# Kernel tuning notes

Hardware: AMD Instinct MI355X
Metric: run time of the kernel (lower is better)

Reference implementation:

```python
import jax, jax.numpy as jnp
import numpy as np

B, IN_DIM, EXP_DIM, E = 16384, 256, 128, 8  # batch, input_dim, expert_dim, expert_num


def setup_inputs() -> dict:
    key = jax.random.key(0)
    ks = jax.random.split(key, 12)
    s_in = 1.0 / np.sqrt(IN_DIM)
    return {
        "x_a": jax.random.normal(ks[0], (B, IN_DIM), jnp.float32),
        "x_b": jax.random.normal(ks[1], (B, IN_DIM), jnp.float32),
        "x_share": jax.random.normal(ks[2], (B, IN_DIM), jnp.float32),
        # expert banks: [E, IN_DIM, EXP_DIM] weights, [E, EXP_DIM] bias
        "Wa": jax.random.uniform(ks[3], (E, IN_DIM, EXP_DIM), jnp.float32, -s_in, s_in),
        "ba": jax.random.uniform(ks[4], (E, EXP_DIM), jnp.float32, -s_in, s_in),
        "Wb": jax.random.uniform(ks[5], (E, IN_DIM, EXP_DIM), jnp.float32, -s_in, s_in),
        "bb": jax.random.uniform(ks[6], (E, EXP_DIM), jnp.float32, -s_in, s_in),
        "Ws": jax.random.uniform(ks[7], (E, IN_DIM, EXP_DIM), jnp.float32, -s_in, s_in),
        "bs": jax.random.uniform(ks[8], (E, EXP_DIM), jnp.float32, -s_in, s_in),
        # gate projections (bias=False): num single-output linears == one [num, IN_DIM] matrix
        "Ga": jax.random.uniform(ks[9], (2 * E, IN_DIM), jnp.float32, -s_in, s_in),
        "Gb": jax.random.uniform(ks[10], (2 * E, IN_DIM), jnp.float32, -s_in, s_in),
        "Gs": jax.random.uniform(ks[11], (3 * E, IN_DIM), jnp.float32, -s_in, s_in),
    }


def _experts(x, W, b):
    # batched dense stack: [B,IN] x [E,IN,D] -> [B,E,D]
    return jnp.einsum("bi,eid->bed", x, W) + b[None, :, :]


def _gate(x, G, experts):
    # logits [B, num]; softmax over experts; weighted sum over expert axis
    w = jax.nn.softmax(x @ G.T, axis=1)
    return jnp.einsum("be,bed->bd", w, experts)


def reference(x_a, x_b, x_share, Wa, ba, Wb, bb, Ws, bs, Ga, Gb, Gs):
    ea = _experts(x_a, Wa, ba)          # [B,E,D]
    eb = _experts(x_b, Wb, bb)          # [B,E,D]
    es = _experts(x_share, Ws, bs)      # [B,E,D]
    out_a = _gate(x_a, Ga, jnp.concatenate([ea, es], axis=1))
    out_b = _gate(x_b, Gb, jnp.concatenate([eb, es], axis=1))
    out_s = _gate(x_share, Gs, jnp.concatenate([ea, eb, es], axis=1))
    return (out_a, out_b, out_s)
```

## Files before the change

kernel.cpp:

```cpp
#include <hip/hip_runtime.h>
#include <stdint.h>

#define BATCH 16384
#define INDIM 256
#define DDIM  128
#define NEXP  8
#define ROWS  64
#define THREADS 512
#define NH    48
#define SLABE 16384

typedef __bf16 bfv8  __attribute__((ext_vector_type(8)));
typedef float  f32x4 __attribute__((ext_vector_type(4)));

typedef __attribute__((address_space(1))) const void gas_void;
typedef __attribute__((address_space(3))) void las_void;

__global__ void prep_kernel(const float* __restrict__ Wa, const float* __restrict__ Wb,
                            const float* __restrict__ Ws, const float* __restrict__ Ga,
                            const float* __restrict__ Gb, const float* __restrict__ Gs,
                            __bf16* __restrict__ wp, __bf16* __restrict__ gp) {
    int t = blockIdx.x * 256 + threadIdx.x;
    const int NW = 3 * 8 * 8 * 8 * 64;
    if (t < NW) {
        int lane = t & 63, nt = (t >> 6) & 7, kt = (t >> 9) & 7, e = (t >> 12) & 7, st = t >> 15;
        const float* W = (st == 0) ? Wa : (st == 1) ? Wb : Ws;
        int d  = nt * 16 + (lane & 15);
        int i0 = kt * 32 + (lane >> 4) * 8;
        __bf16* o = wp + (size_t)t * 8;
#pragma unroll
        for (int j = 0; j < 8; j++)
            o[j] = (__bf16)W[(size_t)(e * 256 + i0 + j) * 128 + d];
    } else if (t < NW + 2048) {
        int t2 = t - NW;
        int lane = t2 & 63, nt = (t2 >> 6) & 3, kt = t2 >> 8;
        int g  = nt * 16 + (lane & 15);
        int k0 = kt * 32 + (lane >> 4) * 8;
        __bf16* o = gp + (size_t)t2 * 8;
#pragma unroll
        for (int j = 0; j < 8; j++) {
            int k = k0 + j;
            float v = 0.f;
            if (g < 16)      v = Ga[g * 256 + k];
            else if (g < 32) v = Gb[(g - 16) * 256 + k];
            else if (g < 56) v = Gs[(g - 32) * 256 + k];
            o[j] = (__bf16)v;
        }
    }
}

__device__ __forceinline__ void load_afr(const float* __restrict__ x, int rb,
                                         int l16, int quad, bfv8 afr[2][8]) {
#pragma unroll
    for (int mt = 0; mt < 2; mt++) {
        const float* xr = x + (size_t)(rb + mt * 16 + l16) * INDIM;
#pragma unroll
        for (int kt = 0; kt < 8; kt++) {
            const f32x4* p = (const f32x4*)(xr + kt * 32 + quad * 8);
            f32x4 lo = __builtin_nontemporal_load(p);
            f32x4 hi = __builtin_nontemporal_load(p + 1);
            bfv8 a;
            a[0] = (__bf16)lo[0]; a[1] = (__bf16)lo[1]; a[2] = (__bf16)lo[2]; a[3] = (__bf16)lo[3];
            a[4] = (__bf16)hi[0]; a[5] = (__bf16)hi[1]; a[6] = (__bf16)hi[2]; a[7] = (__bf16)hi[3];
            afr[mt][kt] = a;
        }
    }
}

__device__ __forceinline__ void stage_half(const __bf16* __restrict__ wp,
                                           __bf16* ring, int h, int wv, int lane) {
    const __bf16* src = wp + ((size_t)h << 14) + (wv << 11) + (lane << 3);
    __bf16* dst = ring + ((h & 1) << 14) + (wv << 11);
#pragma unroll
    for (int i = 0; i < 4; i++)
        __builtin_amdgcn_global_load_lds((gas_void*)(src + (i << 9)),
                                         (las_void*)(dst + (i << 9)), 16, 0, 0);
}

__launch_bounds__(THREADS, 2)
__global__ void ple_kernel(const float* __restrict__ xa, const float* __restrict__ xb,
                           const float* __restrict__ xs,
                           const float* __restrict__ ba, const float* __restrict__ bb,
                           const float* __restrict__ bs,
                           const __bf16* __restrict__ wp, const __bf16* __restrict__ gp,
                           float* __restrict__ out) {
    __shared__ __bf16 ring[2 * SLABE];
    __shared__ float lgt[ROWS * 64];
    __shared__ float wT[64 * ROWS];

    const int tid  = threadIdx.x;
    const int wv   = tid >> 6;
    const int lane = tid & 63;
    const int rg   = wv >> 2;
    const int cg   = wv & 3;
    const int quad = lane >> 4;
    const int l16  = lane & 15;
    const int r0   = blockIdx.x * ROWS;
    const int rb   = r0 + rg * 32;

    stage_half(wp, ring, 0, wv, lane);

    bfv8 afr[2][8];

    {
        const float* x = (cg == 0) ? xa : (cg == 1) ? xb : xs;
        load_afr(x, rb, l16, quad, afr);
        f32x4 acc1[2];
#pragma unroll
        for (int mt = 0; mt < 2; mt++) { f32x4 z = {0.f, 0.f, 0.f, 0.f}; acc1[mt] = z; }
#pragma unroll
        for (int kt = 0; kt < 8; kt++) {
            bfv8 gfr = *(const bfv8*)(gp + ((size_t)(kt * 4 + cg) * 64 + lane) * 8);
#pragma unroll
            for (int mt = 0; mt < 2; mt++)
                acc1[mt] = __builtin_amdgcn_mfma_f32_16x16x32_bf16(afr[mt][kt], gfr, acc1[mt], 0, 0, 0);
        }
#pragma unroll
        for (int mt = 0; mt < 2; mt++)
#pragma unroll
            for (int r = 0; r < 4; r++)
                lgt[(rg * 32 + mt * 16 + quad * 4 + r) * 64 + cg * 16 + l16] = acc1[mt][r];
    }
    __syncthreads();

    if (tid < ROWS) {
        const float* L = lgt + tid * 64;
#pragma unroll
        for (int gi = 0; gi < 3; gi++) {
            const int base = (gi == 0) ? 0 : (gi == 1 ? 16 : 32);
            const int cnt  = (gi == 2) ? 24 : 16;
            float m = -1e30f;
            for (int k = 0; k < cnt; k++) m = fmaxf(m, L[base + k]);
            float s = 0.f;
            for (int k = 0; k < cnt; k++) s += __expf(L[base + k] - m);
            float inv = 1.f / s;
            for (int k = 0; k < cnt; k++) wT[(base + k) * ROWS + tid] = __expf(L[base + k] - m) * inv;
        }
    }
    __syncthreads();

    float o[3][2][2][4];
#pragma unroll
    for (int oi = 0; oi < 3; oi++)
#pragma unroll
        for (int mt = 0; mt < 2; mt++)
#pragma unroll
            for (int ntl = 0; ntl < 2; ntl++)
#pragma unroll
                for (int r = 0; r < 4; r++) o[oi][mt][ntl][r] = 0.f;

#define FOLD(oi, gbase)                                                                 \
    {                                                                                   \
        _Pragma("unroll")                                                               \
        for (int mt = 0; mt < 2; mt++) {                                                \
            f32x4 gw4 = *(const f32x4*)(wT + (gbase + eb) * ROWS + rg * 32 + mt * 16 + quad * 4); \
            _Pragma("unroll")                                                           \
            for (int ntl = 0; ntl < 2; ntl++)                                           \
                _Pragma("unroll")                                                       \
                for (int r = 0; r < 4; r++)                                             \
                    o[oi][mt][ntl][r] += gw4[r] * acc[mt][ntl][r];                      \
        }                                                                               \
    }

#pragma unroll
    for (int st = 0; st < 3; st++) {
        const float* x    = (st == 0) ? xa : (st == 1) ? xb : xs;
        const float* bias = (st == 0) ? ba : (st == 1) ? bb : bs;
        load_afr(x, rb, l16, quad, afr);

#pragma unroll 1
        for (int eb = 0; eb < NEXP; eb++) {
            float b0 = bias[eb * 128 + cg * 32 + l16];
            float b1 = bias[eb * 128 + cg * 32 + 16 + l16];

            f32x4 acc[2][2];
#pragma unroll
            for (int mt = 0; mt < 2; mt++)
#pragma unroll
                for (int ntl = 0; ntl < 2; ntl++) { f32x4 z = {0.f, 0.f, 0.f, 0.f}; acc[mt][ntl] = z; }

#pragma unroll
            for (int half = 0; half < 2; half++) {
                const int h = st * 16 + eb * 2 + half;
                __syncthreads();
                if (h + 1 < NH)
                    stage_half(wp, ring, h + 1, wv, lane);

                const __bf16* buf = ring + (half << 14);
#pragma unroll
                for (int kt4 = 0; kt4 < 4; kt4++) {
                    const int kt = half * 4 + kt4;
                    const __bf16* slab = buf + (kt4 << 12) + (cg << 10);
                    bfv8 bv0 = *(const bfv8*)(slab + ((size_t)lane << 3));
                    bfv8 bv1 = *(const bfv8*)(slab + 512 + ((size_t)lane << 3));
                    acc[0][0] = __builtin_amdgcn_mfma_f32_16x16x32_bf16(afr[0][kt], bv0, acc[0][0], 0, 0, 0);
                    acc[1][0] = __builtin_amdgcn_mfma_f32_16x16x32_bf16(afr[1][kt], bv0, acc[1][0], 0, 0, 0);
                    acc[0][1] = __builtin_amdgcn_mfma_f32_16x16x32_bf16(afr[0][kt], bv1, acc[0][1], 0, 0, 0);
                    acc[1][1] = __builtin_amdgcn_mfma_f32_16x16x32_bf16(afr[1][kt], bv1, acc[1][1], 0, 0, 0);
                }
            }

#pragma unroll
            for (int mt = 0; mt < 2; mt++)
#pragma unroll
                for (int r = 0; r < 4; r++) { acc[mt][0][r] += b0; acc[mt][1][r] += b1; }

            if (st == 0)      { FOLD(0, 0);  FOLD(2, 32); }
            else if (st == 1) { FOLD(1, 16); FOLD(2, 40); }
            else              { FOLD(0, 8);  FOLD(1, 24); FOLD(2, 48); }
        }
    }
#undef FOLD

#pragma unroll
    for (int oi = 0; oi < 3; oi++) {
        float* ob = out + (size_t)oi * BATCH * DDIM;
#pragma unroll
        for (int mt = 0; mt < 2; mt++)
#pragma unroll
            for (int r = 0; r < 4; r++) {
                int row = rb + mt * 16 + quad * 4 + r;
#pragma unroll
                for (int ntl = 0; ntl < 2; ntl++)
                    __builtin_nontemporal_store(o[oi][mt][ntl][r],
                        &ob[(size_t)row * DDIM + cg * 32 + ntl * 16 + l16]);
            }
    }
}

extern "C" void kernel_launch(void* const* d_in, const int* in_sizes, int n_in,
                              void* d_out, int out_size, void* d_ws, size_t ws_size,
                              hipStream_t stream) {
    const float* xa = (const float*)d_in[0];
    const float* xb = (const float*)d_in[1];
    const float* xs = (const float*)d_in[2];
    const float* Wa = (const float*)d_in[3];
    const float* ba = (const float*)d_in[4];
    const float* Wb = (const float*)d_in[5];
    const float* bb = (const float*)d_in[6];
    const float* Ws = (const float*)d_in[7];
    const float* bs = (const float*)d_in[8];
    const float* Ga = (const float*)d_in[9];
    const float* Gb = (const float*)d_in[10];
    const float* Gs = (const float*)d_in[11];

    __bf16* wp = (__bf16*)d_ws;
    __bf16* gp = wp + 3 * 8 * 8 * 8 * 64 * 8;

    prep_kernel<<<392, 256, 0, stream>>>(Wa, Wb, Ws, Ga, Gb, Gs, wp, gp);
    ple_kernel<<<BATCH / ROWS, THREADS, 0, stream>>>(xa, xb, xs, ba, bb, bs, wp, gp, (float*)d_out);
}
```

Before: 186.6 us.

## Coalesce weight repack via LDS transpose and rotate expert order per block

Result: faster. 180.7 us (-3.2%).

```diff
diff --git a/kernel.cpp b/kernel.cpp
--- a/kernel.cpp
+++ b/kernel.cpp
@@ -7,7 +7,7 @@
 #define NEXP  8
 #define ROWS  64
 #define THREADS 512
-#define NH    48
+#define NSEQ  48
 #define SLABE 16384
 
 typedef __bf16 bfv8  __attribute__((ext_vector_type(8)));
@@ -20,19 +20,38 @@
                             const float* __restrict__ Ws, const float* __restrict__ Ga,
                             const float* __restrict__ Gb, const float* __restrict__ Gs,
                             __bf16* __restrict__ wp, __bf16* __restrict__ gp) {
-    int t = blockIdx.x * 256 + threadIdx.x;
-    const int NW = 3 * 8 * 8 * 8 * 64;
-    if (t < NW) {
-        int lane = t & 63, nt = (t >> 6) & 7, kt = (t >> 9) & 7, e = (t >> 12) & 7, st = t >> 15;
+    __shared__ float ws[32 * 132];
+    const int b = blockIdx.x, tid = threadIdx.x;
+    if (b < 192) {
+        const int st = b >> 6, e = (b >> 3) & 7, kt = b & 7;
         const float* W = (st == 0) ? Wa : (st == 1) ? Wb : Ws;
-        int d  = nt * 16 + (lane & 15);
-        int i0 = kt * 32 + (lane >> 4) * 8;
-        __bf16* o = wp + (size_t)t * 8;
-#pragma unroll
-        for (int j = 0; j < 8; j++)
-            o[j] = (__bf16)W[(size_t)(e * 256 + i0 + j) * 128 + d];
-    } else if (t < NW + 2048) {
-        int t2 = t - NW;
+        const float* src = W + (size_t)(e * 256 + kt * 32) * 128;
+#pragma unroll
+        for (int k = 0; k < 4; k++) {
+            int idx4 = tid + k * 256;
+            f32x4 v = *(const f32x4*)(src + (size_t)idx4 * 4);
+            int row = idx4 >> 5;
+            int col = (idx4 & 31) << 2;
+            ws[row * 132 + col + 0] = v[0];
+            ws[row * 132 + col + 1] = v[1];
+            ws[row * 132 + col + 2] = v[2];
+            ws[row * 132 + col + 3] = v[3];
+        }
+        __syncthreads();
+        __bf16* o = wp + ((size_t)b << 12);
+#pragma unroll
+        for (int h2 = 0; h2 < 2; h2++) {
+            int base = tid * 2 + h2;
+            int nt = base >> 6, lane = base & 63;
+            int d  = nt * 16 + (lane & 15);
+            int i0 = (lane >> 4) * 8;
+            bfv8 ov;
+#pragma unroll
+            for (int j = 0; j < 8; j++) ov[j] = (__bf16)ws[(i0 + j) * 132 + d];
+            *(bfv8*)(o + (size_t)base * 8) = ov;
+        }
+    } else {
+        int t2 = (b - 192) * 256 + tid;
         int lane = t2 & 63, nt = (t2 >> 6) & 3, kt = t2 >> 8;
         int g  = nt * 16 + (lane & 15);
         int k0 = kt * 32 + (lane >> 4) * 8;
@@ -67,14 +86,21 @@
     }
 }
 
-__device__ __forceinline__ void stage_half(const __bf16* __restrict__ wp,
-                                           __bf16* ring, int h, int wv, int lane) {
-    const __bf16* src = wp + ((size_t)h << 14) + (wv << 11) + (lane << 3);
-    __bf16* dst = ring + ((h & 1) << 14) + (wv << 11);
+__device__ __forceinline__ void stage_slab(const __bf16* __restrict__ wp,
+                                           __bf16* ring, int hslab, int slot,
+                                           int wv, int lane) {
+    const __bf16* src = wp + ((size_t)hslab << 14) + (wv << 11) + (lane << 3);
+    __bf16* dst = ring + (slot << 14) + (wv << 11);
 #pragma unroll
     for (int i = 0; i < 4; i++)
         __builtin_amdgcn_global_load_lds((gas_void*)(src + (i << 9)),
                                          (las_void*)(dst + (i << 9)), 16, 0, 0);
+}
+
+__device__ __forceinline__ int slab_of(int s, int rot) {
+    int st = s >> 4, r = s & 15;
+    int eb = (((r >> 1) + rot) & 7);
+    return (st << 4) | (eb << 1) | (s & 1);
 }
 
 __launch_bounds__(THREADS, 2)
@@ -97,8 +123,9 @@
     const int l16  = lane & 15;
     const int r0   = blockIdx.x * ROWS;
     const int rb   = r0 + rg * 32;
-
-    stage_half(wp, ring, 0, wv, lane);
+    const int rot  = (blockIdx.x >> 3) & 7;
+
+    stage_slab(wp, ring, slab_of(0, rot), 0, wv, lane);
 
     bfv8 afr[2][8];
 
@@ -169,7 +196,8 @@
         load_afr(x, rb, l16, quad, afr);
 
 #pragma unroll 1
-        for (int eb = 0; eb < NEXP; eb++) {
+        for (int eb0 = 0; eb0 < NEXP; eb0++) {
+            const int eb = (eb0 + rot) & 7;
             float b0 = bias[eb * 128 + cg * 32 + l16];
             float b1 = bias[eb * 128 + cg * 32 + 16 + l16];
 
@@ -181,10 +209,10 @@
 
 #pragma unroll
             for (int half = 0; half < 2; half++) {
-                const int h = st * 16 + eb * 2 + half;
+                const int s = st * 16 + eb0 * 2 + half;
                 __syncthreads();
-                if (h + 1 < NH)
-                    stage_half(wp, ring, h + 1, wv, lane);
+                if (s + 1 < NSEQ)
+                    stage_slab(wp, ring, slab_of(s + 1, rot), (s + 1) & 1, wv, lane);
 
                 const __bf16* buf = ring + (half << 14);
 #pragma unroll
@@ -247,6 +275,6 @@
     __bf16* wp = (__bf16*)d_ws;
     __bf16* gp = wp + 3 * 8 * 8 * 8 * 64 * 8;
 
-    prep_kernel<<<392, 256, 0, stream>>>(Wa, Wb, Ws, Ga, Gb, Gs, wp, gp);
+    prep_kernel<<<200, 256, 0, stream>>>(Wa, Wb, Ws, Ga, Gb, Gs, wp, gp);
     ple_kernel<<<BATCH / ROWS, THREADS, 0, stream>>>(xa, xb, xs, ba, bb, bs, wp, gp, (float*)d_out);
 }
```
